# Kernel tuning notes

Hardware: AMD Instinct MI355X
Metric: run time of the kernel (lower is better)

## Reference

```python
import jax, jax.numpy as jnp
import numpy as np

N = 20000   # nodes per branch
E = 320000  # edges per branch
B = 64      # graphs in batch
DT = 768    # text in_dim
DP = 128    # prop in_dim
H = 256     # hid_dim
O = 128     # out_dim
EPS = 1e-5
SLOPE = 0.01
NUM_REL = 2


def _init_conv(key, din, dout):
    k1, k2 = jax.random.split(key)
    s = 1.0 / np.sqrt(din)
    w_rel = jax.random.uniform(k1, (NUM_REL, din, dout), minval=-s, maxval=s, dtype=jnp.float32)
    w_root = jax.random.uniform(k2, (din, dout), minval=-s, maxval=s, dtype=jnp.float32)
    bias = jnp.zeros((dout,), jnp.float32)
    return w_rel, w_root, bias


def setup_inputs() -> dict:
    key = jax.random.key(0)
    ks = jax.random.split(key, 16)
    inp = {}
    inp["x_t"] = jax.random.normal(ks[0], (N, DT), jnp.float32)
    inp["x_p"] = jax.random.normal(ks[1], (N, DP), jnp.float32)
    inp["edge_index_t"] = jax.random.randint(ks[2], (2, E), 0, N)
    inp["edge_type_t"] = jax.random.randint(ks[3], (E,), 0, NUM_REL)
    inp["x_t_batch"] = jnp.sort(jax.random.randint(ks[4], (N,), 0, B))
    inp["edge_index_p"] = jax.random.randint(ks[5], (2, E), 0, N)
    inp["edge_type_p"] = jax.random.randint(ks[6], (E,), 0, NUM_REL)
    inp["x_p_batch"] = jnp.sort(jax.random.randint(ks[7], (N,), 0, B))
    inp["w_t1_rel"], inp["w_t1_root"], inp["b_t1"] = _init_conv(ks[8], DT, H)
    inp["w_t2_rel"], inp["w_t2_root"], inp["b_t2"] = _init_conv(ks[9], H, O)
    inp["w_p1_rel"], inp["w_p1_root"], inp["b_p1"] = _init_conv(ks[10], DP, H)
    inp["w_p2_rel"], inp["w_p2_root"], inp["b_p2"] = _init_conv(ks[11], H, O)
    inp["g_t1"] = jnp.ones((H,), jnp.float32); inp["be_t1"] = jnp.zeros((H,), jnp.float32)
    inp["g_t2"] = jnp.ones((O,), jnp.float32); inp["be_t2"] = jnp.zeros((O,), jnp.float32)
    inp["g_p1"] = jnp.ones((H,), jnp.float32); inp["be_p1"] = jnp.zeros((H,), jnp.float32)
    inp["g_p2"] = jnp.ones((O,), jnp.float32); inp["be_p2"] = jnp.zeros((O,), jnp.float32)
    return inp


def rgcn_conv(x, edge_index, edge_type, w_rel, w_root, bias):
    # PyG RGCNConv: per-relation mean aggregation of W_r x_j, plus root + bias
    src, dst = edge_index[0], edge_index[1]
    out = x @ w_root + bias
    for r in range(NUM_REL):
        h = x @ w_rel[r]                                   # [N, dout]
        mask = (edge_type == r)
        msg = jnp.where(mask[:, None], h[src], 0.0)        # [E, dout]
        s = jax.ops.segment_sum(msg, dst, num_segments=x.shape[0])
        cnt = jax.ops.segment_sum(mask.astype(x.dtype), dst, num_segments=x.shape[0])
        out = out + s / jnp.maximum(cnt, 1.0)[:, None]
    return out


def batchnorm(x, gamma, beta):
    mu = x.mean(0)
    var = x.var(0)  # biased, matching torch normalization
    return (x - mu) * jax.lax.rsqrt(var + EPS) * gamma + beta


def leaky_relu(x):
    return jnp.where(x >= 0, x, SLOPE * x)


def scatter_mean_pool(x, batch, num_graphs):
    s = jax.ops.segment_sum(x, batch, num_segments=num_graphs)
    cnt = jax.ops.segment_sum(jnp.ones((x.shape[0],), x.dtype), batch, num_segments=num_graphs)
    return s / jnp.maximum(cnt, 1.0)[:, None]


def reference(x_t, x_p,
              w_t1_rel, w_t1_root, b_t1, w_t2_rel, w_t2_root, b_t2,
              w_p1_rel, w_p1_root, b_p1, w_p2_rel, w_p2_root, b_p2,
              g_t1, be_t1, g_t2, be_t2, g_p1, be_p1, g_p2, be_p2,
              edge_index_t, edge_type_t, x_t_batch,
              edge_index_p, edge_type_p, x_p_batch):
    h = rgcn_conv(x_t, edge_index_t, edge_type_t, w_t1_rel, w_t1_root, b_t1)
    h = leaky_relu(batchnorm(h, g_t1, be_t1))
    h = rgcn_conv(h, edge_index_t, edge_type_t, w_t2_rel, w_t2_root, b_t2)
    h = leaky_relu(batchnorm(h, g_t2, be_t2))
    out_t = scatter_mean_pool(h, x_t_batch, B)

    h = rgcn_conv(x_p, edge_index_p, edge_type_p, w_p1_rel, w_p1_root, b_p1)
    h = leaky_relu(batchnorm(h, g_p1, be_p1))
    h = rgcn_conv(h, edge_index_p, edge_type_p, w_p2_rel, w_p2_root, b_p2)
    h = leaky_relu(batchnorm(h, g_p2, be_p2))
    out_p = scatter_mean_pool(h, x_p_batch, B)
    return (out_t, out_p)
```

## Files before the change

kernel.cpp:

```cpp
#include <hip/hip_runtime.h>

#define NN 20000
#define NE 320000
#define NB 64
#define BNG 128

typedef __attribute__((ext_vector_type(4))) float f32x4;
typedef __attribute__((ext_vector_type(8))) __bf16 bf16x8;

static __device__ __forceinline__ ushort f2bf(float f) {
    uint u = __builtin_bit_cast(uint, f);
    uint r = (u + 0x7fffu + ((u >> 16) & 1u)) >> 16;
    return (ushort)r;
}
static __device__ __forceinline__ float bf2f(ushort u) {
    return __builtin_bit_cast(float, (uint)u << 16);
}

#define GLD_LDS16(g, l)                                                                     \
    __builtin_amdgcn_global_load_lds((__attribute__((address_space(1))) void*)(g),          \
                                     (__attribute__((address_space(3))) void*)(l), 16, 0, 0)

struct WtJob { const float* root; const float* rel; ushort* dst; int K; int C; };
struct FillArgs { const int* ei_t; const int* et_t; const int* ei_p; const int* et_p;
                  const int* off; const int* posArr; int* adj; };


__global__ __launch_bounds__(256) void k_prep(const int* __restrict__ ei_t, const int* __restrict__ ei_p,
                                              int* __restrict__ deg, int* __restrict__ posArr,
                                              const float* __restrict__ xt, const float* __restrict__ xp,
                                              ushort* __restrict__ ot, ushort* __restrict__ op,
                                              int n4t, int n4p,
                                              WtJob j0, WtJob j1, WtJob j2, WtJob j3,
                                              int c1, int c2, int c3, int nbCount, int nbCast) {
    __shared__ float tile[32][33];
    int bid = blockIdx.x;
    int tid = threadIdx.x;
    if (bid < nbCount) {
        int e = bid * 256 + tid;
        if (e >= 2 * NE) return;
        int br = e >= NE;
        int el = e - br * NE;
        const int* ei = br ? ei_p : ei_t;
        int dst = ei[NE + el];
        posArr[e] = atomicAdd(&deg[br * NN + dst], 1);
        return;
    }
    if (bid < nbCount + nbCast) {
        int i = (bid - nbCount) * 256 + tid;
        const float* in; ushort* out; int j;
        if (i < n4t) { in = xt; out = ot; j = i; }
        else { j = i - n4t; if (j >= n4p) return; in = xp; out = op; }
        float4 v = *(const float4*)&in[(size_t)j * 4];
        ushort4 o;
        o.x = f2bf(v.x); o.y = f2bf(v.y); o.z = f2bf(v.z); o.w = f2bf(v.w);
        *(ushort4*)&out[(size_t)j * 4] = o;
        return;
    }
    int lt0 = bid - nbCount - nbCast;
    WtJob j; int lt;
    if (lt0 < c1) { j = j0; lt = lt0; }
    else if (lt0 < c2) { j = j1; lt = lt0 - c1; }
    else if (lt0 < c3) { j = j2; lt = lt0 - c2; }
    else { j = j3; lt = lt0 - c3; }
    int nx = j.K >> 5, ny = j.C >> 5;
    int mat = lt / (nx * ny);
    int r2 = lt - mat * (nx * ny);
    int kx = r2 % nx, cy = r2 / nx;
    int KC = j.K * j.C;
    const float* W = (mat == 0) ? j.root : j.rel + (size_t)(mat - 1) * KC;
    int k0 = kx * 32, c0 = cy * 32;
    int tx = tid & 31, ty = tid >> 5;
#pragma unroll
    for (int i = 0; i < 4; i++)
        tile[ty + i * 8][tx] = W[(size_t)(k0 + ty + i * 8) * j.C + c0 + tx];
    __syncthreads();
#pragma unroll
    for (int i = 0; i < 4; i++)
        j.dst[(size_t)mat * KC + (size_t)(c0 + ty + i * 8) * j.K + k0 + tx] = f2bf(tile[tx][ty + i * 8]);
}


__global__ __launch_bounds__(256) void k_scan_local(const int* __restrict__ deg, int* __restrict__ off,
                                                    int* __restrict__ csum, int n) {
    __shared__ int sh[256];
    int base = blockIdx.x * 256, tid = threadIdx.x;
    int v = (base + tid < n) ? deg[base + tid] : 0;
    sh[tid] = v; __syncthreads();
    for (int o = 1; o < 256; o <<= 1) {
        int t = (tid >= o) ? sh[tid - o] : 0;
        __syncthreads();
        sh[tid] += t;
        __syncthreads();
    }
    if (base + tid < n) off[base + tid] = sh[tid] - v;
    if (tid == 255) csum[blockIdx.x] = sh[255];
}

__global__ void k_scan_csum(int* __restrict__ csum, int* __restrict__ offN, int nc) {
    __shared__ int sh[256];
    int tid = threadIdx.x;
    int v = (tid < nc) ? csum[tid] : 0;
    sh[tid] = v; __syncthreads();
    for (int o = 1; o < 256; o <<= 1) {
        int t = (tid >= o) ? sh[tid - o] : 0;
        __syncthreads();
        sh[tid] += t;
        __syncthreads();
    }
    if (tid < nc) csum[tid] = sh[tid] - v;
    if (tid == 255) offN[0] = sh[255];
}

__global__ __launch_bounds__(256) void k_scan_add(int* __restrict__ off, const int* __restrict__ csum, int n) {
    int i = blockIdx.x * 256 + threadIdx.x;
    if (i < n) off[i] += csum[blockIdx.x];
}


struct GemmJob { const ushort* A; const ushort* Wt; const float* bias;
                 ushort* root; ushort* h0; ushort* h1; int K; };

__global__ __launch_bounds__(256, 3) void k_gemm_fill(GemmJob j0, GemmJob j1, int M, int C, int NBR,
                                                      int nwgG, FillArgs fa) {
    __shared__ ushort smem[20480];

    if ((int)blockIdx.x >= nwgG) {
        int e = ((int)blockIdx.x - nwgG) * 256 + threadIdx.x;
        if (e >= 2 * NE) return;
        int br = e >= NE;
        int el = e - br * NE;
        const int* ei = br ? fa.ei_p : fa.ei_t;
        const int* et = br ? fa.et_p : fa.et_t;
        int src = ei[el], dst = ei[NE + el], r = et[el];
        int g = br * NN + dst;
        fa.adj[fa.off[g] + fa.posArr[e]] = src | (r << 28);
        return;
    }

    int nx = C >> 6;
    int perY = nx * NBR;
    int orig = blockIdx.x;
    int q = nwgG >> 3, r = nwgG & 7;
    int xcd = orig & 7, pos = orig >> 3;
    int wgid = (xcd < r) ? (xcd * (q + 1) + pos) : (r * (q + 1) + (xcd - r) * q + pos);
    int y = wgid / perY, rem = wgid - y * perY;
    int br = rem / nx, x = rem - br * nx;
    GemmJob j = br ? j1 : j0;
    int K = j.K;

    int tid = threadIdx.x;
    int lane = tid & 63, wave = tid >> 6;
    int wr = wave >> 1, wc = wave & 1;
    int rowTile = y * 128, colTile = x * 64;

    f32x4 acc[3][4][2] = {};

    for (int k0 = 0; k0 < K; k0 += 64) {
        __syncthreads();
#pragma unroll
        for (int i = 0; i < 4; i++) {
            int id = i * 256 + tid;
            int rr = id >> 3, ck = id & 7;
            int garow = rowTile + rr;
            if (garow >= M) garow = M - 1;
            GLD_LDS16(j.A + (size_t)garow * K + k0 + ck * 8, &smem[id * 8]);
        }
#pragma unroll
        for (int z = 0; z < 3; z++) {
            const ushort* Bz = j.Wt + (size_t)z * C * K;
#pragma unroll
            for (int i = 0; i < 2; i++) {
                int id = i * 256 + tid;
                int rr = id >> 3, ck = id & 7;
                GLD_LDS16(Bz + (size_t)(colTile + rr) * K + k0 + ck * 8,
                          &smem[8192 + z * 4096 + id * 8]);
            }
        }
        __syncthreads();
#pragma unroll
        for (int kk = 0; kk < 2; kk++) {
            int kb = kk * 32 + (lane >> 4) * 8;
            bf16x8 af[4];
#pragma unroll
            for (int mi = 0; mi < 4; mi++)
                af[mi] = *(const bf16x8*)&smem[(wr * 64 + mi * 16 + (lane & 15)) * 64 + kb];
#pragma unroll
            for (int z = 0; z < 3; z++) {
                bf16x8 bfr[2];
#pragma unroll
                for (int ni = 0; ni < 2; ni++)
                    bfr[ni] = *(const bf16x8*)&smem[8192 + z * 4096 +
                                                    (wc * 32 + ni * 16 + (lane & 15)) * 64 + kb];
#pragma unroll
                for (int mi = 0; mi < 4; mi++)
#pragma unroll
                    for (int ni = 0; ni < 2; ni++)
                        acc[z][mi][ni] =
                            __builtin_amdgcn_mfma_f32_16x16x32_bf16(af[mi], bfr[ni], acc[z][mi][ni], 0, 0, 0);
            }
        }
    }

    int lc = lane & 15, lr4 = (lane >> 4) * 4;
#pragma unroll
    for (int z = 0; z < 3; z++) {
        ushort* H = (z == 0) ? j.root : (z == 1 ? j.h0 : j.h1);
        __syncthreads();
#pragma unroll
        for (int ni = 0; ni < 2; ni++) {
            int cl = wc * 32 + ni * 16 + lc;
            float bj = (z == 0) ? j.bias[colTile + cl] : 0.f;
#pragma unroll
            for (int mi = 0; mi < 4; mi++)
#pragma unroll
                for (int jj = 0; jj < 4; jj++) {
                    int rloc = wr * 64 + mi * 16 + lr4 + jj;
                    int chunk = (cl >> 3) ^ (rloc & 7);
                    smem[rloc * 64 + (chunk << 3) + (cl & 7)] = f2bf(acc[z][mi][ni][jj] + bj);
                }
        }
        __syncthreads();
#pragma unroll
        for (int it = 0; it < 4; it++) {
            int cid = it * 256 + tid;
            int rloc = cid >> 3, cc = cid & 7;
            int grow = rowTile + rloc;
            if (grow < M) {
                int4 v = *(const int4*)&smem[rloc * 64 + ((cc ^ (rloc & 7)) << 3)];
                *(int4*)&H[(size_t)grow * C + colTile + cc * 8] = v;
            }
        }
    }
}


__global__ __launch_bounds__(256) void k_agg256(const int* __restrict__ off, const int* __restrict__ adj,
                                                const ushort* __restrict__ h0t, const ushort* __restrict__ h1t,
                                                const ushort* __restrict__ roott, ushort* __restrict__ vt,
                                                const ushort* __restrict__ h0p, const ushort* __restrict__ h1p,
                                                const ushort* __restrict__ rootp, ushort* __restrict__ vp,
                                                int perBr) {
    __shared__ float4 shA[2][64];
    __shared__ float4 shB[2][64];
    __shared__ int shc[2][2];
    int br = blockIdx.x >= perBr;
    int bb = blockIdx.x - br * perBr;
    const int* offb = off + br * NN;
    const ushort* h0 = br ? h0p : h0t;
    const ushort* h1 = br ? h1p : h1t;
    const ushort* root = br ? rootp : roott;
    ushort* vout = br ? vp : vt;
    int wave = threadIdx.x >> 6, lane = threadIdx.x & 63;
    int nb = wave >> 1, w = wave & 1;
    int node = bb * 2 + nb;
    int s = offb[node], e = offb[node + 1];
    int len = e - s;
    int mid = s + ((len + 1) >> 1);
    int i0 = w ? mid : s;
    int i1 = w ? e : mid;
    float4 a0 = make_float4(0.f, 0.f, 0.f, 0.f);
    float4 a1 = make_float4(0.f, 0.f, 0.f, 0.f);
    float4 b0 = make_float4(0.f, 0.f, 0.f, 0.f);
    float4 b1 = make_float4(0.f, 0.f, 0.f, 0.f);
    int c0 = 0, c1 = 0;
    int i = i0;
    for (; i + 1 < i1; i += 2) {
        int v0 = adj[i], v1 = adj[i + 1];
        int s0 = v0 & 0x0FFFFFFF, r0 = v0 >> 28;
        int s1 = v1 & 0x0FFFFFFF, r1 = v1 >> 28;
        const ushort* hp0 = r0 ? h1 : h0;
        const ushort* hp1 = r1 ? h1 : h0;
        ushort4 x0 = *(const ushort4*)&hp0[(size_t)s0 * 256 + lane * 4];
        ushort4 x1 = *(const ushort4*)&hp1[(size_t)s1 * 256 + lane * 4];
        if (r0) { a1.x += bf2f(x0.x); a1.y += bf2f(x0.y); a1.z += bf2f(x0.z); a1.w += bf2f(x0.w); c1++; }
        else    { a0.x += bf2f(x0.x); a0.y += bf2f(x0.y); a0.z += bf2f(x0.z); a0.w += bf2f(x0.w); c0++; }
        if (r1) { b1.x += bf2f(x1.x); b1.y += bf2f(x1.y); b1.z += bf2f(x1.z); b1.w += bf2f(x1.w); c1++; }
        else    { b0.x += bf2f(x1.x); b0.y += bf2f(x1.y); b0.z += bf2f(x1.z); b0.w += bf2f(x1.w); c0++; }
    }
    if (i < i1) {
        int v0 = adj[i];
        int s0 = v0 & 0x0FFFFFFF, r0 = v0 >> 28;
        const ushort* hp0 = r0 ? h1 : h0;
        ushort4 x0 = *(const ushort4*)&hp0[(size_t)s0 * 256 + lane * 4];
        if (r0) { a1.x += bf2f(x0.x); a1.y += bf2f(x0.y); a1.z += bf2f(x0.z); a1.w += bf2f(x0.w); c1++; }
        else    { a0.x += bf2f(x0.x); a0.y += bf2f(x0.y); a0.z += bf2f(x0.z); a0.w += bf2f(x0.w); c0++; }
    }
    float4 s0v = make_float4(a0.x + b0.x, a0.y + b0.y, a0.z + b0.z, a0.w + b0.w);
    float4 s1v = make_float4(a1.x + b1.x, a1.y + b1.y, a1.z + b1.z, a1.w + b1.w);
    if (w) {
        shA[nb][lane] = s0v; shB[nb][lane] = s1v;
        if (lane == 0) { shc[nb][0] = c0; shc[nb][1] = c1; }
    }
    __syncthreads();
    if (!w) {
        float4 t0 = shA[nb][lane], t1 = shB[nb][lane];
        c0 += shc[nb][0]; c1 += shc[nb][1];
        float w0 = 1.0f / (float)(c0 > 0 ? c0 : 1);
        float w1 = 1.0f / (float)(c1 > 0 ? c1 : 1);
        ushort4 rt = *(const ushort4*)&root[(size_t)node * 256 + lane * 4];
        ushort4 o;
        o.x = f2bf(bf2f(rt.x) + (s0v.x + t0.x) * w0 + (s1v.x + t1.x) * w1);
        o.y = f2bf(bf2f(rt.y) + (s0v.y + t0.y) * w0 + (s1v.y + t1.y) * w1);
        o.z = f2bf(bf2f(rt.z) + (s0v.z + t0.z) * w0 + (s1v.z + t1.z) * w1);
        o.w = f2bf(bf2f(rt.w) + (s0v.w + t0.w) * w0 + (s1v.w + t1.w) * w1);
        *(ushort4*)&vout[(size_t)node * 256 + lane * 4] = o;
    }
}

__global__ __launch_bounds__(256) void k_agg128(const int* __restrict__ offAll, const int* __restrict__ adj,
                                                const ushort* __restrict__ h0t, const ushort* __restrict__ h1t,
                                                const ushort* __restrict__ roott, ushort* __restrict__ vt,
                                                const ushort* __restrict__ h0p, const ushort* __restrict__ h1p,
                                                const ushort* __restrict__ rootp, ushort* __restrict__ vp) {
    int half = gridDim.x >> 1;
    int br = blockIdx.x >= half;
    int bb = blockIdx.x - br * half;
    int wave = threadIdx.x >> 6, lane = threadIdx.x & 63;
    int node = bb * 4 + wave;
    const int* off = offAll + br * NN;
    const ushort* h0 = br ? h0p : h0t;
    const ushort* h1 = br ? h1p : h1t;
    const ushort* root = br ? rootp : roott;
    ushort* vout = br ? vp : vt;
    int s = off[node], e = off[node + 1];
    int l32 = lane & 31, ep = lane >> 5;
    float4 a0 = make_float4(0.f, 0.f, 0.f, 0.f);
    float4 a1 = make_float4(0.f, 0.f, 0.f, 0.f);
    float4 b0 = make_float4(0.f, 0.f, 0.f, 0.f);
    float4 b1 = make_float4(0.f, 0.f, 0.f, 0.f);
    int c0 = 0, c1 = 0;
    int i = s + ep;
    for (; i + 2 < e; i += 4) {
        int v0 = adj[i], v1 = adj[i + 2];
        int s0 = v0 & 0x0FFFFFFF, r0 = v0 >> 28;
        int s1 = v1 & 0x0FFFFFFF, r1 = v1 >> 28;
        const ushort* hp0 = r0 ? h1 : h0;
        const ushort* hp1 = r1 ? h1 : h0;
        ushort4 x0 = *(const ushort4*)&hp0[(size_t)s0 * 128 + l32 * 4];
        ushort4 x1 = *(const ushort4*)&hp1[(size_t)s1 * 128 + l32 * 4];
        if (r0) { a1.x += bf2f(x0.x); a1.y += bf2f(x0.y); a1.z += bf2f(x0.z); a1.w += bf2f(x0.w); c1++; }
        else    { a0.x += bf2f(x0.x); a0.y += bf2f(x0.y); a0.z += bf2f(x0.z); a0.w += bf2f(x0.w); c0++; }
        if (r1) { b1.x += bf2f(x1.x); b1.y += bf2f(x1.y); b1.z += bf2f(x1.z); b1.w += bf2f(x1.w); c1++; }
        else    { b0.x += bf2f(x1.x); b0.y += bf2f(x1.y); b0.z += bf2f(x1.z); b0.w += bf2f(x1.w); c0++; }
    }
    if (i < e) {
        int v0 = adj[i];
        int s0 = v0 & 0x0FFFFFFF, r0 = v0 >> 28;
        const ushort* hp0 = r0 ? h1 : h0;
        ushort4 x0 = *(const ushort4*)&hp0[(size_t)s0 * 128 + l32 * 4];
        if (r0) { a1.x += bf2f(x0.x); a1.y += bf2f(x0.y); a1.z += bf2f(x0.z); a1.w += bf2f(x0.w); c1++; }
        else    { a0.x += bf2f(x0.x); a0.y += bf2f(x0.y); a0.z += bf2f(x0.z); a0.w += bf2f(x0.w); c0++; }
    }
    float sx0 = a0.x + b0.x, sy0 = a0.y + b0.y, sz0 = a0.z + b0.z, sw0 = a0.w + b0.w;
    float sx1 = a1.x + b1.x, sy1 = a1.y + b1.y, sz1 = a1.z + b1.z, sw1 = a1.w + b1.w;
    sx0 += __shfl_xor(sx0, 32); sy0 += __shfl_xor(sy0, 32);
    sz0 += __shfl_xor(sz0, 32); sw0 += __shfl_xor(sw0, 32);
    sx1 += __shfl_xor(sx1, 32); sy1 += __shfl_xor(sy1, 32);
    sz1 += __shfl_xor(sz1, 32); sw1 += __shfl_xor(sw1, 32);
    c0 += __shfl_xor(c0, 32); c1 += __shfl_xor(c1, 32);
    if (ep == 0) {
        float w0 = 1.0f / (float)(c0 > 0 ? c0 : 1);
        float w1 = 1.0f / (float)(c1 > 0 ? c1 : 1);
        ushort4 rt = *(const ushort4*)&root[(size_t)node * 128 + l32 * 4];
        ushort4 o;
        o.x = f2bf(bf2f(rt.x) + sx0 * w0 + sx1 * w1);
        o.y = f2bf(bf2f(rt.y) + sy0 * w0 + sy1 * w1);
        o.z = f2bf(bf2f(rt.z) + sz0 * w0 + sz1 * w1);
        o.w = f2bf(bf2f(rt.w) + sw0 * w0 + sw1 * w1);
        *(ushort4*)&vout[(size_t)node * 128 + l32 * 4] = o;
    }
}


__global__ __launch_bounds__(256) void k_bnstats(const ushort* __restrict__ v0buf, const ushort* __restrict__ v1buf,
                                                 float* __restrict__ part, int C, int M) {
    int br = blockIdx.y;
    const ushort* v = br ? v1buf : v0buf;
    float* P = part + (size_t)br * 2 * C * BNG;
    int tid = threadIdx.x;
    int half = C >> 1;
    int groups = 256 / half;
    int col2 = tid & (half - 1);
    int rg = tid / half;
    float sx = 0.f, sy = 0.f, qx = 0.f, qy = 0.f;
    for (int row = blockIdx.x * groups + rg; row < M; row += BNG * groups) {
        uint rv = *(const uint*)&v[(size_t)row * C + col2 * 2];
        float v0 = bf2f((ushort)(rv & 0xffff));
        float v1 = bf2f((ushort)(rv >> 16));
        sx += v0; qx += v0 * v0;
        sy += v1; qy += v1 * v1;
    }
    __shared__ float4 sh[256];
    sh[tid] = make_float4(sx, sy, qx, qy);
    __syncthreads();
    if (tid < half) {
        float4 a = sh[tid];
        for (int g = 1; g < groups; g++) {
            float4 b = sh[tid + g * half];
            a.x += b.x; a.y += b.y; a.z += b.z; a.w += b.w;
        }
        int c0 = tid * 2;
        P[(size_t)c0 * BNG + blockIdx.x] = a.x;
        P[(size_t)(c0 + 1) * BNG + blockIdx.x] = a.y;
        P[(size_t)(C + c0) * BNG + blockIdx.x] = a.z;
        P[(size_t)(C + c0 + 1) * BNG + blockIdx.x] = a.w;
    }
}

__global__ __launch_bounds__(256) void k_bnreduce(const float* __restrict__ part,
                                                  const float* __restrict__ g0, const float* __restrict__ be0,
                                                  const float* __restrict__ g1, const float* __restrict__ be1,
                                                  float* __restrict__ ss, int C, float invM) {
    int br = blockIdx.y;
    const float* P = part + (size_t)br * 2 * C * BNG;
    const float* g = br ? g1 : g0;
    const float* be = br ? be1 : be0;
    float* S = ss + br * 2 * C;
    int wv = threadIdx.x >> 6, lane = threadIdx.x & 63;
    int c = blockIdx.x * 4 + wv;
    if (c >= C) return;
    float s = P[(size_t)c * BNG + lane] + P[(size_t)c * BNG + 64 + lane];
    float s2 = P[(size_t)(C + c) * BNG + lane] + P[(size_t)(C + c) * BNG + 64 + lane];
#pragma unroll
    for (int o = 32; o >= 1; o >>= 1) {
        s += __shfl_xor(s, o, 64);
        s2 += __shfl_xor(s2, o, 64);
    }
    if (lane == 0) {
        float mu = s * invM;
        float var = s2 * invM - mu * mu;
        float sc = g[c] * rsqrtf(var + 1e-5f);
        S[c] = sc;
        S[C + c] = be[c] - mu * sc;
    }
}

__global__ __launch_bounds__(256) void k_bnapply(const ushort* __restrict__ v0buf, const ushort* __restrict__ v1buf,
                                                 const float* __restrict__ ss, int C, int M,
                                                 ushort* __restrict__ ob0, ushort* __restrict__ ob1) {
    int br = blockIdx.y;
    const ushort* v = br ? v1buf : v0buf;
    const float* S = ss + br * 2 * C;
    int i = blockIdx.x * 256 + threadIdx.x;
    int total4 = M * C / 4;
    if (i >= total4) return;
    ushort4 vv = *(const ushort4*)&v[(size_t)i * 4];
    int c0 = (i * 4) & (C - 1);
    float y0 = bf2f(vv.x) * S[c0 + 0] + S[C + c0 + 0];
    float y1 = bf2f(vv.y) * S[c0 + 1] + S[C + c0 + 1];
    float y2 = bf2f(vv.z) * S[c0 + 2] + S[C + c0 + 2];
    float y3 = bf2f(vv.w) * S[c0 + 3] + S[C + c0 + 3];
    y0 = y0 >= 0.f ? y0 : 0.01f * y0;
    y1 = y1 >= 0.f ? y1 : 0.01f * y1;
    y2 = y2 >= 0.f ? y2 : 0.01f * y2;
    y3 = y3 >= 0.f ? y3 : 0.01f * y3;
    ushort* ob = br ? ob1 : ob0;
    ushort4 o;
    o.x = f2bf(y0); o.y = f2bf(y1); o.z = f2bf(y2); o.w = f2bf(y3);
    *(ushort4*)&ob[(size_t)i * 4] = o;
}


__global__ __launch_bounds__(512) void k_pool2(const ushort* __restrict__ v2t, const ushort* __restrict__ v2p,
                                               const int* __restrict__ bt, const int* __restrict__ bp,
                                               const float* __restrict__ ss, float* __restrict__ out) {
    int blk = blockIdx.x;
    int br = blk >> 6, b = blk & 63;
    const ushort* v = br ? v2p : v2t;
    const int* bat = br ? bp : bt;
    const float* S = ss + br * 2 * 128;
    __shared__ int se[2];
    if (threadIdx.x < 2) {
        int val = b + (int)threadIdx.x;
        int lo = 0, hi = NN;
        while (lo < hi) {
            int mid = (lo + hi) >> 1;
            if (bat[mid] < val) lo = mid + 1; else hi = mid;
        }
        se[threadIdx.x] = lo;
    }
    __syncthreads();
    int s = se[0], e = se[1];
    int t2 = threadIdx.x & 63, rg = threadIdx.x >> 6;
    float sc0 = S[t2 * 2], sh0 = S[128 + t2 * 2];
    float sc1 = S[t2 * 2 + 1], sh1 = S[128 + t2 * 2 + 1];
    float ax = 0.f, ay = 0.f;
    for (int r = s + rg; r < e; r += 8) {
        uint rv = *(const uint*)&v[(size_t)r * 128 + t2 * 2];
        float v0 = bf2f((ushort)(rv & 0xffff)) * sc0 + sh0;
        float v1 = bf2f((ushort)(rv >> 16)) * sc1 + sh1;
        v0 = v0 >= 0.f ? v0 : 0.01f * v0;
        v1 = v1 >= 0.f ? v1 : 0.01f * v1;
        ax += v0; ay += v1;
    }
    __shared__ float2 sh[512];
    sh[threadIdx.x] = make_float2(ax, ay);
    __syncthreads();
    if (rg == 0) {
        float2 a = sh[t2];
#pragma unroll
        for (int g = 1; g < 8; g++) {
            float2 vv = sh[t2 + g * 64];
            a.x += vv.x; a.y += vv.y;
        }
        int cnt = e - s;
        float inv = 1.0f / (float)(cnt > 0 ? cnt : 1);
        out[(br * 64 + b) * 128 + t2 * 2] = a.x * inv;
        out[(br * 64 + b) * 128 + t2 * 2 + 1] = a.y * inv;
    }
}


extern "C" void kernel_launch(void* const* d_in, const int* in_sizes, int n_in,
                              void* d_out, int out_size, void* d_ws, size_t ws_size,
                              hipStream_t stream) {
    const float* x_t = (const float*)d_in[0];
    const float* x_p = (const float*)d_in[1];
    const int* ei_t = (const int*)d_in[2];
    const int* et_t = (const int*)d_in[3];
    const int* bat_t = (const int*)d_in[4];
    const int* ei_p = (const int*)d_in[5];
    const int* et_p = (const int*)d_in[6];
    const int* bat_p = (const int*)d_in[7];
    const float* w_t1_rel = (const float*)d_in[8];
    const float* w_t1_root = (const float*)d_in[9];
    const float* b_t1 = (const float*)d_in[10];
    const float* w_t2_rel = (const float*)d_in[11];
    const float* w_t2_root = (const float*)d_in[12];
    const float* b_t2 = (const float*)d_in[13];
    const float* w_p1_rel = (const float*)d_in[14];
    const float* w_p1_root = (const float*)d_in[15];
    const float* b_p1 = (const float*)d_in[16];
    const float* w_p2_rel = (const float*)d_in[17];
    const float* w_p2_root = (const float*)d_in[18];
    const float* b_p2 = (const float*)d_in[19];
    const float* g_t1 = (const float*)d_in[20]; const float* be_t1 = (const float*)d_in[21];
    const float* g_t2 = (const float*)d_in[22]; const float* be_t2 = (const float*)d_in[23];
    const float* g_p1 = (const float*)d_in[24]; const float* be_p1 = (const float*)d_in[25];
    const float* g_p2 = (const float*)d_in[26]; const float* be_p2 = (const float*)d_in[27];

    char* wp = (char*)d_ws;
    auto alloc = [&](size_t b) -> void* {
        void* p = (void*)wp;
        wp += (b + 255) & ~(size_t)255;
        return p;
    };

    const bool MERGED = ws_size >= (size_t)137 * 1000 * 1000;

    dim3 blk(256);
    const int EB2 = (2 * NE) / 256;
    const int SCB2 = (2 * NN + 255) / 256;
    const int nMT = (NN + 127) / 128;

    ushort* xt_bf; ushort* xp_bf;
    ushort *h0t1, *h1t1, *h0p1, *h1p1;
    ushort *root1t, *v1t, *root1p, *v1p;
    ushort *a1t, *a1p;
    ushort *root2t, *v2t, *root2p, *v2p;
    ushort *h0t2, *h1t2, *h0p2, *h1p2;
    ushort* wtb; int* adj; int* posArr; int* off; int* deg; int* csum;
    float* part; float* ss;

    if (MERGED) {
        xt_bf = (ushort*)alloc((size_t)NN * 768 * 2);
        xp_bf = (ushort*)alloc((size_t)NN * 128 * 2);
        h0t1 = (ushort*)alloc((size_t)NN * 256 * 2);
        h1t1 = (ushort*)alloc((size_t)NN * 256 * 2);
        h0p1 = (ushort*)alloc((size_t)NN * 256 * 2);
        h1p1 = (ushort*)alloc((size_t)NN * 256 * 2);
        root1t = (ushort*)alloc((size_t)NN * 256 * 2);
        v1t = (ushort*)alloc((size_t)NN * 256 * 2);
        root1p = (ushort*)alloc((size_t)NN * 256 * 2);
        v1p = (ushort*)alloc((size_t)NN * 256 * 2);
        a1t = (ushort*)alloc((size_t)NN * 256 * 2);
        wtb = (ushort*)alloc((size_t)(3 * 768 * 256 + 3 * 128 * 256 + 2 * 3 * 256 * 128) * 2);
        adj = (int*)alloc((size_t)2 * NE * 4);
        posArr = (int*)alloc((size_t)2 * NE * 4);
        off = (int*)alloc((size_t)(2 * NN + 1) * 4);
        deg = (int*)alloc((size_t)2 * NN * 4);
        csum = (int*)alloc(256 * 4);
        part = (float*)alloc((size_t)2 * 2 * 256 * BNG * 4);
        ss = (float*)alloc(1024 * 4);
        root2t = xt_bf;
        v2t = root2t + (size_t)NN * 128;
        root2p = v2t + (size_t)NN * 128;
        v2p = root2p + (size_t)NN * 128;
        a1p = v2p + (size_t)NN * 128;
        h0t2 = h0t1;                       h0p2 = h0t1 + (size_t)NN * 128;
        h1t2 = h1t1;                       h1p2 = h1t1 + (size_t)NN * 128;
    } else {
        xt_bf = (ushort*)alloc((size_t)NN * 768 * 2);
        xp_bf = (ushort*)alloc((size_t)NN * 128 * 2);
        ushort* h0b = (ushort*)alloc((size_t)NN * 256 * 2);
        ushort* h1b = (ushort*)alloc((size_t)NN * 256 * 2);
        ushort* root1 = (ushort*)alloc((size_t)NN * 256 * 2);
        ushort* v1 = (ushort*)alloc((size_t)NN * 256 * 2);
        a1t = (ushort*)alloc((size_t)NN * 256 * 2);
        wtb = (ushort*)alloc((size_t)(3 * 768 * 256 + 3 * 128 * 256 + 2 * 3 * 256 * 128) * 2);
        adj = (int*)alloc((size_t)2 * NE * 4);
        posArr = (int*)alloc((size_t)2 * NE * 4);
        off = (int*)alloc((size_t)(2 * NN + 1) * 4);
        deg = (int*)alloc((size_t)2 * NN * 4);
        csum = (int*)alloc(256 * 4);
        part = (float*)alloc((size_t)2 * 2 * 256 * BNG * 4);
        ss = (float*)alloc(1024 * 4);
        h0t1 = h0b; h1t1 = h1b; h0p1 = h0b; h1p1 = h1b;
        root1t = root1; v1t = v1; root1p = root1; v1p = v1;
        root2t = xt_bf;
        v2t = root2t + (size_t)NN * 128;
        root2p = v2t + (size_t)NN * 128;
        v2p = root2p + (size_t)NN * 128;
        a1p = v2p + (size_t)NN * 128;
        h0t2 = h0b;                        h0p2 = h0b + (size_t)NN * 128;
        h1t2 = h1b;                        h1p2 = h1b + (size_t)NN * 128;
    }

    ushort* wt_t1 = wtb;
    ushort* wt_p1 = wt_t1 + 3 * 768 * 256;
    ushort* wt_t2 = wt_p1 + 3 * 128 * 256;
    ushort* wt_p2 = wt_t2 + 3 * 256 * 128;
    WtJob j0 = {w_t1_root, w_t1_rel, wt_t1, 768, 256};
    WtJob j1 = {w_p1_root, w_p1_rel, wt_p1, 128, 256};
    WtJob j2 = {w_t2_root, w_t2_rel, wt_t2, 256, 128};
    WtJob j3 = {w_p2_root, w_p2_rel, wt_p2, 256, 128};

    int n4t = NN * 768 / 4, n4p = NN * 128 / 4;
    int nbCast = (n4t + n4p + 255) / 256;

    hipMemsetAsync(deg, 0, (size_t)2 * NN * 4, stream);
    k_prep<<<EB2 + nbCast + 864, blk, 0, stream>>>(ei_t, ei_p, deg, posArr,
                                                   x_t, x_p, xt_bf, xp_bf, n4t, n4p,
                                                   j0, j1, j2, j3, 576, 672, 768, EB2, nbCast);
    k_scan_local<<<SCB2, blk, 0, stream>>>(deg, off, csum, 2 * NN);
    k_scan_csum<<<1, 256, 0, stream>>>(csum, off + 2 * NN, SCB2);
    k_scan_add<<<SCB2, blk, 0, stream>>>(off, csum, 2 * NN);

    FillArgs fa = {ei_t, et_t, ei_p, et_p, off, posArr, adj};
    GemmJob Gt1 = {xt_bf, wt_t1, b_t1, root1t, h0t1, h1t1, 768};
    GemmJob Gp1 = {xp_bf, wt_p1, b_p1, root1p, h0p1, h1p1, 128};

    if (MERGED) {
        int nwgG = nMT * 4 * 2;
        k_gemm_fill<<<nwgG + EB2, blk, 0, stream>>>(Gt1, Gp1, NN, 256, 2, nwgG, fa);
        k_agg256<<<NN, blk, 0, stream>>>(off, adj, h0t1, h1t1, root1t, v1t,
                                         h0p1, h1p1, root1p, v1p, NN / 2);
        k_bnstats<<<dim3(BNG, 2), blk, 0, stream>>>(v1t, v1p, part, 256, NN);
        k_bnreduce<<<dim3(64, 2), blk, 0, stream>>>(part, g_t1, be_t1, g_p1, be_p1, ss, 256, 1.0f / NN);
        k_bnapply<<<dim3((NN * 256 / 4 + 255) / 256, 2), blk, 0, stream>>>(
            v1t, v1p, ss, 256, NN, a1t, a1p);
    } else {
        int nwgG = nMT * 4;
        k_gemm_fill<<<nwgG + EB2, blk, 0, stream>>>(Gt1, Gt1, NN, 256, 1, nwgG, fa);
        k_agg256<<<NN / 2, blk, 0, stream>>>(off, adj, h0t1, h1t1, root1t, v1t,
                                             h0t1, h1t1, root1t, v1t, NN / 2);
        k_bnstats<<<dim3(BNG, 1), blk, 0, stream>>>(v1t, v1t, part, 256, NN);
        k_bnreduce<<<dim3(64, 1), blk, 0, stream>>>(part, g_t1, be_t1, g_t1, be_t1, ss, 256, 1.0f / NN);
        k_bnapply<<<dim3((NN * 256 / 4 + 255) / 256, 1), blk, 0, stream>>>(
            v1t, v1t, ss, 256, NN, a1t, a1t);

        k_gemm_fill<<<nwgG, blk, 0, stream>>>(Gp1, Gp1, NN, 256, 1, nwgG, fa);
        k_agg256<<<NN / 2, blk, 0, stream>>>(off + NN, adj, h0p1, h1p1, root1p, v1p,
                                             h0p1, h1p1, root1p, v1p, NN / 2);
        k_bnstats<<<dim3(BNG, 1), blk, 0, stream>>>(v1p, v1p, part, 256, NN);
        k_bnreduce<<<dim3(64, 1), blk, 0, stream>>>(part, g_p1, be_p1, g_p1, be_p1, ss, 256, 1.0f / NN);
        k_bnapply<<<dim3((NN * 256 / 4 + 255) / 256, 1), blk, 0, stream>>>(
            v1p, v1p, ss, 256, NN, a1p, a1p);
    }

    GemmJob Gt2 = {a1t, wt_t2, b_t2, root2t, h0t2, h1t2, 256};
    GemmJob Gp2 = {a1p, wt_p2, b_p2, root2p, h0p2, h1p2, 256};
    int nwg2 = nMT * 2 * 2;
    k_gemm_fill<<<nwg2, blk, 0, stream>>>(Gt2, Gp2, NN, 128, 2, nwg2, fa);
    k_agg128<<<2 * (NN / 4), blk, 0, stream>>>(off, adj, h0t2, h1t2, root2t, v2t,
                                               h0p2, h1p2, root2p, v2p);
    k_bnstats<<<dim3(BNG, 2), blk, 0, stream>>>(v2t, v2p, part, 128, NN);
    k_bnreduce<<<dim3(32, 2), blk, 0, stream>>>(part, g_t2, be_t2, g_p2, be_p2, ss, 128, 1.0f / NN);

    k_pool2<<<128, 512, 0, stream>>>(v2t, v2p, bat_t, bat_p, ss, (float*)d_out);
}
```

Measured before the change: 280.9 us.

## Split GEMM tiles per weight matrix and load B fragments directly from global

The fused GEMM now gives each workgroup one of the three weight matrices (root, rel0, rel1) over a 128x128 output tile, instead of all three matrices over a 64-column tile. B fragments are read straight from global memory into registers rather than staged through LDS. This cuts LDS use and accumulator registers so more workgroups fit per CU. The cost is that the A tile is loaded three times as often and B reads are unstaged, uncoalesced row reads.

```diff
diff --git a/kernel.cpp b/kernel.cpp
--- a/kernel.cpp
+++ b/kernel.cpp
@@ -121,9 +121,9 @@
 struct GemmJob { const ushort* A; const ushort* Wt; const float* bias;
                  ushort* root; ushort* h0; ushort* h1; int K; };
 
-__global__ __launch_bounds__(256, 3) void k_gemm_fill(GemmJob j0, GemmJob j1, int M, int C, int NBR,
+__global__ __launch_bounds__(256, 4) void k_gemm_fill(GemmJob j0, GemmJob j1, int M, int C, int NBR,
                                                       int nwgG, FillArgs fa) {
-    __shared__ ushort smem[20480];
+    __shared__ ushort smem[16384];
 
     if ((int)blockIdx.x >= nwgG) {
         int e = ((int)blockIdx.x - nwgG) * 256 + threadIdx.x;
@@ -138,23 +138,30 @@
         return;
     }
 
-    int nx = C >> 6;
-    int perY = nx * NBR;
+    int nx = C >> 7;
+    int perY = nx * 3 * NBR;
     int orig = blockIdx.x;
     int q = nwgG >> 3, r = nwgG & 7;
     int xcd = orig & 7, pos = orig >> 3;
     int wgid = (xcd < r) ? (xcd * (q + 1) + pos) : (r * (q + 1) + (xcd - r) * q + pos);
     int y = wgid / perY, rem = wgid - y * perY;
-    int br = rem / nx, x = rem - br * nx;
+    int x = rem / (3 * NBR), zz = rem - x * (3 * NBR);
+    int br = zz / 3, z = zz - br * 3;
     GemmJob j = br ? j1 : j0;
     int K = j.K;
 
+    const ushort* B = j.Wt + (size_t)z * C * K;
     int tid = threadIdx.x;
     int lane = tid & 63, wave = tid >> 6;
     int wr = wave >> 1, wc = wave & 1;
-    int rowTile = y * 128, colTile = x * 64;
-
-    f32x4 acc[3][4][2] = {};
+    int rowTile = y * 128, colTile = x * 128;
+
+    const ushort* Brow[4];
+#pragma unroll
+    for (int ni = 0; ni < 4; ni++)
+        Brow[ni] = B + (size_t)(colTile + wc * 64 + ni * 16 + (lane & 15)) * K;
+
+    f32x4 acc[4][4] = {};
 
     for (int k0 = 0; k0 < K; k0 += 64) {
         __syncthreads();
@@ -166,70 +173,50 @@
             if (garow >= M) garow = M - 1;
             GLD_LDS16(j.A + (size_t)garow * K + k0 + ck * 8, &smem[id * 8]);
         }
-#pragma unroll
-        for (int z = 0; z < 3; z++) {
-            const ushort* Bz = j.Wt + (size_t)z * C * K;
-#pragma unroll
-            for (int i = 0; i < 2; i++) {
-                int id = i * 256 + tid;
-                int rr = id >> 3, ck = id & 7;
-                GLD_LDS16(Bz + (size_t)(colTile + rr) * K + k0 + ck * 8,
-                          &smem[8192 + z * 4096 + id * 8]);
-            }
-        }
         __syncthreads();
 #pragma unroll
         for (int kk = 0; kk < 2; kk++) {
             int kb = kk * 32 + (lane >> 4) * 8;
-            bf16x8 af[4];
+            bf16x8 af[4], bfr[4];
 #pragma unroll
             for (int mi = 0; mi < 4; mi++)
                 af[mi] = *(const bf16x8*)&smem[(wr * 64 + mi * 16 + (lane & 15)) * 64 + kb];
 #pragma unroll
-            for (int z = 0; z < 3; z++) {
-                bf16x8 bfr[2];
-#pragma unroll
-                for (int ni = 0; ni < 2; ni++)
-                    bfr[ni] = *(const bf16x8*)&smem[8192 + z * 4096 +
-                                                    (wc * 32 + ni * 16 + (lane & 15)) * 64 + kb];
-#pragma unroll
-                for (int mi = 0; mi < 4; mi++)
-#pragma unroll
-                    for (int ni = 0; ni < 2; ni++)
-                        acc[z][mi][ni] =
-                            __builtin_amdgcn_mfma_f32_16x16x32_bf16(af[mi], bfr[ni], acc[z][mi][ni], 0, 0, 0);
+            for (int ni = 0; ni < 4; ni++)
+                bfr[ni] = *(const bf16x8*)&Brow[ni][k0 + kb];
+#pragma unroll
+            for (int mi = 0; mi < 4; mi++)
+#pragma unroll
+                for (int ni = 0; ni < 4; ni++)
+                    acc[mi][ni] = __builtin_amdgcn_mfma_f32_16x16x32_bf16(af[mi], bfr[ni], acc[mi][ni], 0, 0, 0);
+        }
+    }
+
+    int lc = lane & 15, lr4 = (lane >> 4) * 4;
+    ushort* H = (z == 0) ? j.root : (z == 1 ? j.h0 : j.h1);
+    __syncthreads();
+#pragma unroll
+    for (int ni = 0; ni < 4; ni++) {
+        int col = wc * 64 + ni * 16 + lc;
+        float bj = (z == 0) ? j.bias[colTile + col] : 0.f;
+#pragma unroll
+        for (int mi = 0; mi < 4; mi++)
+#pragma unroll
+            for (int jj = 0; jj < 4; jj++) {
+                int rloc = wr * 64 + mi * 16 + lr4 + jj;
+                int chunk = (col >> 3) ^ (rloc & 7);
+                smem[rloc * 128 + (chunk << 3) + (col & 7)] = f2bf(acc[mi][ni][jj] + bj);
             }
-        }
-    }
-
-    int lc = lane & 15, lr4 = (lane >> 4) * 4;
-#pragma unroll
-    for (int z = 0; z < 3; z++) {
-        ushort* H = (z == 0) ? j.root : (z == 1 ? j.h0 : j.h1);
-        __syncthreads();
-#pragma unroll
-        for (int ni = 0; ni < 2; ni++) {
-            int cl = wc * 32 + ni * 16 + lc;
-            float bj = (z == 0) ? j.bias[colTile + cl] : 0.f;
-#pragma unroll
-            for (int mi = 0; mi < 4; mi++)
-#pragma unroll
-                for (int jj = 0; jj < 4; jj++) {
-                    int rloc = wr * 64 + mi * 16 + lr4 + jj;
-                    int chunk = (cl >> 3) ^ (rloc & 7);
-                    smem[rloc * 64 + (chunk << 3) + (cl & 7)] = f2bf(acc[z][mi][ni][jj] + bj);
-                }
-        }
-        __syncthreads();
-#pragma unroll
-        for (int it = 0; it < 4; it++) {
-            int cid = it * 256 + tid;
-            int rloc = cid >> 3, cc = cid & 7;
-            int grow = rowTile + rloc;
-            if (grow < M) {
-                int4 v = *(const int4*)&smem[rloc * 64 + ((cc ^ (rloc & 7)) << 3)];
-                *(int4*)&H[(size_t)grow * C + colTile + cc * 8] = v;
-            }
+    }
+    __syncthreads();
+#pragma unroll
+    for (int it = 0; it < 8; it++) {
+        int cid = it * 256 + tid;
+        int rloc = cid >> 4, cc = cid & 15;
+        int grow = rowTile + rloc;
+        if (grow < M) {
+            int4 v = *(const int4*)&smem[rloc * 128 + ((cc ^ (rloc & 7)) << 3)];
+            *(int4*)&H[(size_t)grow * C + colTile + cc * 8] = v;
         }
     }
 }
@@ -642,7 +629,7 @@
     GemmJob Gp1 = {xp_bf, wt_p1, b_p1, root1p, h0p1, h1p1, 128};
 
     if (MERGED) {
-        int nwgG = nMT * 4 * 2;
+        int nwgG = nMT * 2 * 3 * 2;
         k_gemm_fill<<<nwgG + EB2, blk, 0, stream>>>(Gt1, Gp1, NN, 256, 2, nwgG, fa);
         k_agg256<<<NN, blk, 0, stream>>>(off, adj, h0t1, h1t1, root1t, v1t,
                                          h0p1, h1p1, root1p, v1p, NN / 2);
@@ -651,7 +638,7 @@
         k_bnapply<<<dim3((NN * 256 / 4 + 255) / 256, 2), blk, 0, stream>>>(
             v1t, v1p, ss, 256, NN, a1t, a1p);
     } else {
-        int nwgG = nMT * 4;
+        int nwgG = nMT * 2 * 3;
         k_gemm_fill<<<nwgG + EB2, blk, 0, stream>>>(Gt1, Gt1, NN, 256, 1, nwgG, fa);
         k_agg256<<<NN / 2, blk, 0, stream>>>(off, adj, h0t1, h1t1, root1t, v1t,
                                              h0t1, h1t1, root1t, v1t, NN / 2);
@@ -671,7 +658,7 @@
 
     GemmJob Gt2 = {a1t, wt_t2, b_t2, root2t, h0t2, h1t2, 256};
     GemmJob Gp2 = {a1p, wt_p2, b_p2, root2p, h0p2, h1p2, 256};
-    int nwg2 = nMT * 2 * 2;
+    int nwg2 = nMT * 1 * 3 * 2;
     k_gemm_fill<<<nwg2, blk, 0, stream>>>(Gt2, Gp2, NN, 128, 2, nwg2, fa);
     k_agg128<<<2 * (NN / 4), blk, 0, stream>>>(off, adj, h0t2, h1t2, root2t, v2t,
                                                h0p2, h1p2, root2p, v2p);
```

Measured after the change: 327.1 us. +16.4%, slower.
